# Kernel optimization log

Hardware: AMD Instinct MI355X
Metric: run time of the kernel (lower is better)

The kernel has to match this reference:

```python
import jax, jax.numpy as jnp
import numpy as np

L, D = 2, 128
NV, NF, E, G = 100000, 100000, 800000, 64


def setup_inputs() -> dict:
    key = jax.random.key(0)
    ks = jax.random.split(key, 16)
    p = lambda k, s: (0.02 * jax.random.normal(k, s)).astype(jnp.float32)
    return {
        "variables": jax.random.normal(ks[0], (NV, D), jnp.float32),
        "factors": jax.random.normal(ks[1], (NF, D), jnp.float32),
        "edge_index": jnp.stack([
            jax.random.randint(ks[2], (E,), 0, NV),
            jax.random.randint(ks[3], (E,), 0, NF),
        ]).astype(jnp.int64 if jax.config.jax_enable_x64 else jnp.int32),
        "edge_attr": jax.random.normal(ks[4], (E,), jnp.float32),
        "batch_idx": jnp.sort(jax.random.randint(ks[5], (NF,), 0, G)),
        "Wm_vf": p(ks[6], (L, 2 * D, D)), "bm_vf": jnp.zeros((L, D), jnp.float32),
        "Wc_vf": p(ks[7], (L, 2 * D, D)), "bc_vf": jnp.zeros((L, D), jnp.float32),
        "Wm_fv": p(ks[8], (L, 2 * D, D)), "bm_fv": jnp.zeros((L, D), jnp.float32),
        "Wc_fv": p(ks[9], (L, 2 * D, D)), "bc_fv": jnp.zeros((L, D), jnp.float32),
        "Wg": p(ks[10], (D, 1)), "bg": jnp.zeros((1,), jnp.float32),
        "Wt": p(ks[11], (D, D)), "bt": jnp.zeros((D,), jnp.float32),
        "Wl": p(ks[12], (2 * D, D)), "bl": jnp.zeros((D,), jnp.float32),
    }


def _mlp(x, W, b):
    # MLPLayer assumed = Linear + activation (relu)
    return jax.nn.relu(x @ W + b)


def reference(variables, factors, edge_index, edge_attr, batch_idx,
              Wm_vf, bm_vf, Wc_vf, bc_vf, Wm_fv, bm_fv, Wc_fv, bc_fv,
              Wg, bg, Wt, bt, Wl, bl):
    src_v = edge_index[0]  # variable index per edge
    dst_f = edge_index[1]  # factor index per edge
    for l in range(L):
        # var -> factor: message MLP(concat[x_i=factor@dst, x_j=var@src]), sum-agg into factors
        m_vf = _mlp(jnp.concatenate([factors[dst_f], variables[src_v]], -1), Wm_vf[l], bm_vf[l])
        aggr_f = jax.ops.segment_sum(m_vf, dst_f, num_segments=NF)
        new_factors = _mlp(jnp.concatenate([factors, aggr_f], -1), Wc_vf[l], bc_vf[l])
        # factor -> var (flipped edges): message MLP(concat[x_i=var@src_v, x_j=factor@dst_f])
        m_fv = _mlp(jnp.concatenate([variables[src_v], factors[dst_f]], -1), Wm_fv[l], bm_fv[l])
        aggr_v = jax.ops.segment_sum(m_fv, src_v, num_segments=NV)
        new_variables = variables + _mlp(jnp.concatenate([variables, aggr_v], -1), Wc_fv[l], bc_fv[l])
        variables, factors = new_variables, new_factors
    # GlobalNode: attentional aggregation over factors, g_prev = zeros
    gate = (factors @ Wg + bg)[:, 0]                                  # [NF]
    seg_max = jax.ops.segment_max(gate, batch_idx, num_segments=G)
    e = jnp.exp(gate - seg_max[batch_idx])
    denom = jax.ops.segment_sum(e, batch_idx, num_segments=G)
    attn = e / denom[batch_idx]                                       # segment softmax
    g_att = jax.ops.segment_sum(attn[:, None] * (factors @ Wt + bt), batch_idx, num_segments=G)
    g_prev = jnp.zeros((G, D), factors.dtype)
    g = g_prev + _mlp(jnp.concatenate([g_att, g_prev], -1), Wl, bl)
    return variables, factors, g
```

## Files before the change

kernel.cpp:

```cpp
#include <hip/hip_runtime.h>
#include <hip/hip_bf16.h>

typedef unsigned short u16;
typedef unsigned int u32;
typedef __attribute__((ext_vector_type(4))) float f32x4;
typedef __attribute__((ext_vector_type(8))) __bf16 bf16x8;

__device__ __forceinline__ u16 f2bf(float f) {
    u32 x = __float_as_uint(f);
    u32 r = x + 0x7fffu + ((x >> 16) & 1u);
    return (u16)(r >> 16);
}
__device__ __forceinline__ float bf2f(u16 u) {
    return __uint_as_float(((u32)u) << 16);
}

__global__ __launch_bounds__(256) void prep_w(
    const float* __restrict__ Wm_vf, const float* __restrict__ Wc_vf,
    const float* __restrict__ Wm_fv, const float* __restrict__ Wc_fv,
    const float* __restrict__ Wtr, u16* __restrict__ dst)
{
    int i = blockIdx.x * 256 + threadIdx.x;
    if (i >= 17 * 16384) return;
    int m = i >> 14;
    int r = i & 16383;
    int c = r >> 7;
    int k = r & 127;
    const float* p;
    if (m == 16) {
        p = Wtr;
    } else {
        int l = m >> 3, j = m & 7;
        const float* base = (j < 2) ? Wm_vf : (j < 4) ? Wm_fv : (j < 6) ? Wc_vf : Wc_fv;
        p = base + l * 32768 + (j & 1) * 16384;
    }
    dst[m * 16384 + c * 128 + k] = f2bf(p[k * 128 + c]);
}

#define EPB 2048

__global__ __launch_bounds__(256) void hist_part(
    const int* __restrict__ es, const int* __restrict__ ed,
    int* __restrict__ cntV, int* __restrict__ cntF,
    int E, int vChunk, int fChunk)
{
    int part = blockIdx.x & 7;
    int base = (blockIdx.x >> 3) * EPB;
    int end = base + EPB < E ? base + EPB : E;
    int vLo = part * vChunk, vHi = vLo + vChunk;
    int fLo = part * fChunk, fHi = fLo + fChunk;
    for (int i = base + threadIdx.x; i < end; i += 256) {
        int v = es[i], f = ed[i];
        if (v >= vLo && v < vHi) atomicAdd(&cntV[v], 1);
        if (f >= fLo && f < fHi) atomicAdd(&cntF[f], 1);
    }
}

__global__ __launch_bounds__(256) void scan1_k(
    const int* __restrict__ cnt, int* __restrict__ rs, int* __restrict__ bsum, int N)
{
    __shared__ int sd[256];
    int t = threadIdx.x;
    int b0 = blockIdx.x * 1024;
    int v[4]; int s = 0;
#pragma unroll
    for (int j = 0; j < 4; j++) { int i = b0 + t * 4 + j; v[j] = (i < N) ? cnt[i] : 0; s += v[j]; }
    sd[t] = s; __syncthreads();
    for (int off = 1; off < 256; off <<= 1) {
        int x = (t >= off) ? sd[t - off] : 0;
        __syncthreads();
        sd[t] += x;
        __syncthreads();
    }
    int excl = sd[t] - s;
    if (t == 255) bsum[blockIdx.x] = sd[255];
    int run = excl;
#pragma unroll
    for (int j = 0; j < 4; j++) { int i = b0 + t * 4 + j; if (i < N) rs[i] = run; run += v[j]; }
}

__global__ __launch_bounds__(256) void scan2_k(int* __restrict__ bsum, int NB)
{
    __shared__ int sd[256];
    int t = threadIdx.x;
    int s = (t < NB) ? bsum[t] : 0;
    sd[t] = s; __syncthreads();
    for (int off = 1; off < 256; off <<= 1) {
        int x = (t >= off) ? sd[t - off] : 0;
        __syncthreads();
        sd[t] += x;
        __syncthreads();
    }
    if (t < NB) bsum[t] = sd[t] - s;
}

__global__ __launch_bounds__(256) void scan3_k(
    int* __restrict__ rs, const int* __restrict__ bsum, int N, int E)
{
    int i = blockIdx.x * 256 + threadIdx.x;
    if (i < N) rs[i] += bsum[i >> 10];
    else if (i == N) rs[N] = E;
}

__global__ __launch_bounds__(256) void fill_part(
    const int* __restrict__ es, const int* __restrict__ ed,
    const int* __restrict__ rsF, const int* __restrict__ rsV,
    int* __restrict__ cntF, int* __restrict__ cntV,
    int* __restrict__ elF, int* __restrict__ elV,
    int E, int vChunk, int fChunk)
{
    int part = blockIdx.x & 7;
    int base = (blockIdx.x >> 3) * EPB;
    int end = base + EPB < E ? base + EPB : E;
    int vLo = part * vChunk, vHi = vLo + vChunk;
    int fLo = part * fChunk, fHi = fLo + fChunk;
    for (int i = base + threadIdx.x; i < end; i += 256) {
        int v = es[i], f = ed[i];
        if (f >= fLo && f < fHi) { int p = rsF[f] + atomicSub(&cntF[f], 1) - 1; elF[p] = v; }
        if (v >= vLo && v < vHi) { int p = rsV[v] + atomicSub(&cntV[v], 1) - 1; elV[p] = f; }
    }
}

__global__ __launch_bounds__(256) void aggregate_k(
    u16* __restrict__ OWN, const u16* __restrict__ OTH,
    const int* __restrict__ rs, const int* __restrict__ el,
    const float* __restrict__ bias, int N)
{
    int row = blockIdx.x * 4 + (threadIdx.x >> 6);
    if (row >= N) return;
    int lane = threadIdx.x & 63;
    int start = rs[row], end = rs[row + 1];
    ushort2 h = *(const ushort2*)&OWN[(size_t)row * 128 + lane * 2];
    float2 bv = *(const float2*)&bias[lane * 2];
    float c0 = bf2f(h.x) + bv.x;
    float c1 = bf2f(h.y) + bv.y;
    float a0 = 0.f, a1 = 0.f;
    for (int p0 = start; p0 < end; p0 += 64) {
        int n = end - p0; if (n > 64) n = 64;
        int myidx = (lane < n) ? el[p0 + lane] : 0;
        int j = 0;
        for (; j + 4 <= n; j += 4) {
            int o0 = __shfl(myidx, j);
            int o1 = __shfl(myidx, j + 1);
            int o2 = __shfl(myidx, j + 2);
            int o3 = __shfl(myidx, j + 3);
            ushort2 b0 = *(const ushort2*)&OTH[(size_t)o0 * 128 + lane * 2];
            ushort2 b1 = *(const ushort2*)&OTH[(size_t)o1 * 128 + lane * 2];
            ushort2 b2 = *(const ushort2*)&OTH[(size_t)o2 * 128 + lane * 2];
            ushort2 b3 = *(const ushort2*)&OTH[(size_t)o3 * 128 + lane * 2];
            a0 += fmaxf(c0 + bf2f(b0.x), 0.f) + fmaxf(c0 + bf2f(b1.x), 0.f)
                + fmaxf(c0 + bf2f(b2.x), 0.f) + fmaxf(c0 + bf2f(b3.x), 0.f);
            a1 += fmaxf(c1 + bf2f(b0.y), 0.f) + fmaxf(c1 + bf2f(b1.y), 0.f)
                + fmaxf(c1 + bf2f(b2.y), 0.f) + fmaxf(c1 + bf2f(b3.y), 0.f);
        }
        for (; j < n; j++) {
            int o = __shfl(myidx, j);
            ushort2 b = *(const ushort2*)&OTH[(size_t)o * 128 + lane * 2];
            a0 += fmaxf(c0 + bf2f(b.x), 0.f);
            a1 += fmaxf(c1 + bf2f(b.y), 0.f);
        }
    }
    ushort2 r; r.x = f2bf(a0); r.y = f2bf(a1);
    *(ushort2*)&OWN[(size_t)row * 128 + lane * 2] = r;
}

template <bool TWO, bool X2BF, bool RELU, bool RES, bool OBF16>
__global__ __launch_bounds__(256) void gemm_k(
    const float* __restrict__ X1, const void* __restrict__ X2,
    const u16* __restrict__ W1, const u16* __restrict__ W2,
    const float* __restrict__ bias, const float* __restrict__ res,
    float* __restrict__ Yf, u16* __restrict__ Yb, int N)
{
    __shared__ __align__(16) u16 Xs[64 * 136];
    __shared__ __align__(16) u16 Ws[128 * 136];
    const int tid = threadIdx.x;
    const int lane = tid & 63;
    const int wv = tid >> 6;
    const int r0 = blockIdx.x * 64;

    f32x4 acc[8];
#pragma unroll
    for (int i = 0; i < 8; i++) acc[i] = (f32x4)0.f;

#pragma unroll
    for (int p = 0; p < (TWO ? 2 : 1); ++p) {
        const u16* __restrict__ W = (TWO && p) ? W2 : W1;
        if (p) __syncthreads();
        if (TWO && p && X2BF) {
            const u16* Xb = (const u16*)X2;
#pragma unroll
            for (int j = 0; j < 4; j++) {
                int q = j * 256 + tid;
                int row = q >> 4;
                int col = (q & 15) * 8;
                uint4 v = make_uint4(0, 0, 0, 0);
                int gr = r0 + row;
                if (gr < N) v = *(const uint4*)&Xb[(size_t)gr * 128 + col];
                *(uint4*)&Xs[row * 136 + col] = v;
            }
        } else {
            const float* __restrict__ X = (TWO && p) ? (const float*)X2 : X1;
#pragma unroll
            for (int j = 0; j < 8; j++) {
                int q = j * 256 + tid;
                int row = q >> 5;
                int col = (q & 31) * 4;
                float4 v = make_float4(0.f, 0.f, 0.f, 0.f);
                int gr = r0 + row;
                if (gr < N) v = *(const float4*)&X[(size_t)gr * 128 + col];
                ushort4 h;
                h.x = f2bf(v.x); h.y = f2bf(v.y); h.z = f2bf(v.z); h.w = f2bf(v.w);
                *(ushort4*)&Xs[row * 136 + col] = h;
            }
        }
#pragma unroll
        for (int j = 0; j < 8; j++) {
            int q = j * 256 + tid;
            int c = q >> 4;
            int k = (q & 15) * 8;
            uint4 w = *(const uint4*)&W[c * 128 + k];
            *(uint4*)&Ws[c * 136 + k] = w;
        }
        __syncthreads();
#pragma unroll
        for (int ks = 0; ks < 4; ks++) {
            bf16x8 a = *(const bf16x8*)&Xs[(wv * 16 + (lane & 15)) * 136 + ks * 32 + (lane >> 4) * 8];
#pragma unroll
            for (int ct = 0; ct < 8; ct++) {
                bf16x8 b = *(const bf16x8*)&Ws[(ct * 16 + (lane & 15)) * 136 + ks * 32 + (lane >> 4) * 8];
                acc[ct] = __builtin_amdgcn_mfma_f32_16x16x32_bf16(a, b, acc[ct], 0, 0, 0);
            }
        }
    }
#pragma unroll
    for (int ct = 0; ct < 8; ct++) {
        int col = ct * 16 + (lane & 15);
        float bv = bias ? bias[col] : 0.f;
#pragma unroll
        for (int r = 0; r < 4; r++) {
            int row = wv * 16 + (lane >> 4) * 4 + r;
            int gr = r0 + row;
            if (gr < N) {
                float v = acc[ct][r] + bv;
                if (RELU) v = fmaxf(v, 0.f);
                if (RES) v += res[(size_t)gr * 128 + col];
                if (OBF16) Yb[(size_t)gr * 128 + col] = f2bf(v);
                else       Yf[(size_t)gr * 128 + col] = v;
            }
        }
    }
}

__global__ __launch_bounds__(256) void gemm_dual(
    const float* __restrict__ X, const u16* __restrict__ W1, const u16* __restrict__ W2,
    u16* __restrict__ Y1, u16* __restrict__ Y2, int N)
{
    __shared__ __align__(16) u16 Xs[64 * 136];
    __shared__ __align__(16) u16 Ws[128 * 136];
    const int tid = threadIdx.x;
    const int lane = tid & 63;
    const int wv = tid >> 6;
    const int r0 = blockIdx.x * 64;

    f32x4 acc1[8], acc2[8];
#pragma unroll
    for (int i = 0; i < 8; i++) { acc1[i] = (f32x4)0.f; acc2[i] = (f32x4)0.f; }

#pragma unroll
    for (int j = 0; j < 8; j++) {
        int q = j * 256 + tid;
        int row = q >> 5;
        int col = (q & 31) * 4;
        float4 v = make_float4(0.f, 0.f, 0.f, 0.f);
        int gr = r0 + row;
        if (gr < N) v = *(const float4*)&X[(size_t)gr * 128 + col];
        ushort4 h;
        h.x = f2bf(v.x); h.y = f2bf(v.y); h.z = f2bf(v.z); h.w = f2bf(v.w);
        *(ushort4*)&Xs[row * 136 + col] = h;
    }
#pragma unroll
    for (int p = 0; p < 2; ++p) {
        const u16* __restrict__ W = p ? W2 : W1;
        if (p) __syncthreads();
#pragma unroll
        for (int j = 0; j < 8; j++) {
            int q = j * 256 + tid;
            int c = q >> 4;
            int k = (q & 15) * 8;
            uint4 w = *(const uint4*)&W[c * 128 + k];
            *(uint4*)&Ws[c * 136 + k] = w;
        }
        __syncthreads();
#pragma unroll
        for (int ks = 0; ks < 4; ks++) {
            bf16x8 a = *(const bf16x8*)&Xs[(wv * 16 + (lane & 15)) * 136 + ks * 32 + (lane >> 4) * 8];
#pragma unroll
            for (int ct = 0; ct < 8; ct++) {
                bf16x8 b = *(const bf16x8*)&Ws[(ct * 16 + (lane & 15)) * 136 + ks * 32 + (lane >> 4) * 8];
                if (p) acc2[ct] = __builtin_amdgcn_mfma_f32_16x16x32_bf16(a, b, acc2[ct], 0, 0, 0);
                else   acc1[ct] = __builtin_amdgcn_mfma_f32_16x16x32_bf16(a, b, acc1[ct], 0, 0, 0);
            }
        }
    }
#pragma unroll
    for (int ct = 0; ct < 8; ct++) {
        int col = ct * 16 + (lane & 15);
#pragma unroll
        for (int r = 0; r < 4; r++) {
            int row = wv * 16 + (lane >> 4) * 4 + r;
            int gr = r0 + row;
            if (gr < N) {
                Y1[(size_t)gr * 128 + col] = f2bf(acc1[ct][r]);
                Y2[(size_t)gr * 128 + col] = f2bf(acc2[ct][r]);
            }
        }
    }
}

__global__ __launch_bounds__(256) void gate_k(
    const float* __restrict__ F, const float* __restrict__ Wg,
    const float* __restrict__ bg, float* __restrict__ gate, int NF)
{
    int lane = threadIdx.x & 63;
    int f = blockIdx.x * 4 + (threadIdx.x >> 6);
    if (f >= NF) return;
    float p = F[(size_t)f * 128 + lane] * Wg[lane]
            + F[(size_t)f * 128 + 64 + lane] * Wg[64 + lane];
#pragma unroll
    for (int off = 32; off; off >>= 1) p += __shfl_down(p, off);
    if (lane == 0) gate[f] = p + bg[0];
}

__global__ __launch_bounds__(256) void gstats_k(
    const float* __restrict__ gate, const int* __restrict__ batch,
    float* __restrict__ mx, float* __restrict__ dn, int NF)
{
    int g = blockIdx.x, tid = threadIdx.x;
    int lo = 0, hi = NF;
    while (lo < hi) { int mid = (lo + hi) >> 1; if (batch[mid] < g) lo = mid + 1; else hi = mid; }
    int start = lo;
    lo = start; hi = NF;
    while (lo < hi) { int mid = (lo + hi) >> 1; if (batch[mid] < g + 1) lo = mid + 1; else hi = mid; }
    int end = lo;

    __shared__ float red[256];
    float m = -3.4e38f;
    for (int i = start + tid; i < end; i += 256) m = fmaxf(m, gate[i]);
    red[tid] = m; __syncthreads();
    for (int s = 128; s; s >>= 1) { if (tid < s) red[tid] = fmaxf(red[tid], red[tid + s]); __syncthreads(); }
    float mval = red[0]; __syncthreads();
    float s = 0.f;
    for (int i = start + tid; i < end; i += 256) s += __expf(gate[i] - mval);
    red[tid] = s; __syncthreads();
    for (int t = 128; t; t >>= 1) { if (tid < t) red[tid] += red[tid + t]; __syncthreads(); }
    if (tid == 0) { mx[g] = mval; dn[g] = red[0]; }
}

__global__ __launch_bounds__(128) void wsum_k(
    const float* __restrict__ gate, const float* __restrict__ T,
    const int* __restrict__ batch, const float* __restrict__ mx,
    const float* __restrict__ dn, float* __restrict__ g_att, int NF)
{
    int tid = threadIdx.x;
    int i0 = blockIdx.x * 256;
    if (i0 >= NF) return;
    int iend = i0 + 256; if (iend > NF) iend = NF;
    int curg = batch[i0];
    float acc = 0.f;
    for (int i = i0; i < iend; i++) {
        int g = batch[i];
        if (g != curg) {
            atomicAdd(&g_att[(size_t)curg * 128 + tid], acc);
            acc = 0.f; curg = g;
        }
        float w = __expf(gate[i] - mx[g]) / dn[g];
        acc += w * T[(size_t)i * 128 + tid];
    }
    atomicAdd(&g_att[(size_t)curg * 128 + tid], acc);
}

__global__ __launch_bounds__(128) void gfinal_k(
    const float* __restrict__ g_att, const float* __restrict__ Wl,
    const float* __restrict__ bl, float* __restrict__ out_g)
{
    int g = blockIdx.x, tid = threadIdx.x;
    __shared__ float ga[128];
    ga[tid] = g_att[(size_t)g * 128 + tid];
    __syncthreads();
    float o = bl[tid];
    for (int k = 0; k < 128; k++) o += ga[k] * Wl[k * 128 + tid];
    out_g[(size_t)g * 128 + tid] = fmaxf(o, 0.f);
}

extern "C" void kernel_launch(void* const* d_in, const int* in_sizes, int n_in,
                              void* d_out, int out_size, void* d_ws, size_t ws_size,
                              hipStream_t stream)
{
    const int D = 128;
    const int NV = in_sizes[0] / D;
    const int NF = in_sizes[1] / D;
    const int E  = in_sizes[2] / 2;
    const int G  = out_size / D - NV - NF;

    const float* vars_in = (const float*)d_in[0];
    const float* facs_in = (const float*)d_in[1];
    const int*   eidx    = (const int*)d_in[2];
    const int*   e_src   = eidx;
    const int*   e_dst   = eidx + E;
    const int*   batch   = (const int*)d_in[4];
    const float* Wm_vf = (const float*)d_in[5],  *bm_vf = (const float*)d_in[6];
    const float* Wc_vf = (const float*)d_in[7],  *bc_vf = (const float*)d_in[8];
    const float* Wm_fv = (const float*)d_in[9],  *bm_fv = (const float*)d_in[10];
    const float* Wc_fv = (const float*)d_in[11], *bc_fv = (const float*)d_in[12];
    const float* Wg  = (const float*)d_in[13], *bg = (const float*)d_in[14];
    const float* Wtr = (const float*)d_in[15], *bt = (const float*)d_in[16];
    const float* Wl  = (const float*)d_in[17], *bl = (const float*)d_in[18];

    char* ws = (char*)d_ws;
    size_t off = 0;
    u16* WB   = (u16*)ws;            off = 1u << 20;
    u16* BUFA = (u16*)(ws + off);    off += (size_t)NF * 256;
    u16* BUFB = (u16*)(ws + off);    off += (size_t)NV * 256;
    u16* BUFC = (u16*)(ws + off);    off += (size_t)NF * 256;
    float* Tbuf = (float*)BUFA;
    int* rsF  = (int*)(ws + off);    off += (size_t)(NF + 1) * 4;
    int* rsV  = (int*)(ws + off);    off += (size_t)(NV + 1) * 4;
    int* cntF = (int*)(ws + off);    off += (size_t)NF * 4;
    int* cntV = (int*)(ws + off);    off += (size_t)NV * 4;
    int* elF  = (int*)(ws + off);    off += (size_t)E * 4;
    int* elV  = (int*)(ws + off);    off += (size_t)E * 4;
    int* bsum = (int*)(ws + off);    off += 4096;
    float* mx    = (float*)(ws + off); off += (size_t)G * 4;
    float* dn    = (float*)(ws + off); off += (size_t)G * 4;
    float* g_att = (float*)(ws + off); off += (size_t)G * 512;
    float* gate  = (float*)(ws + off); off += (size_t)NF * 4;

    float* out_v = (float*)d_out;
    float* out_f = out_v + (size_t)NV * D;
    float* out_g = out_f + (size_t)NF * D;

    prep_w<<<(17 * 16384 + 255) / 256, 256, 0, stream>>>(Wm_vf, Wc_vf, Wm_fv, Wc_fv, Wtr, WB);

    const int vChunk = (NV + 7) / 8, fChunk = (NF + 7) / 8;
    const int CH = (E + EPB - 1) / EPB;
    hipMemsetAsync(cntF, 0, (size_t)(NF + NV) * 4, stream);
    hist_part<<<CH * 8, 256, 0, stream>>>(e_src, e_dst, cntV, cntF, E, vChunk, fChunk);
    const int NBf = (NF + 1023) / 1024, NBv = (NV + 1023) / 1024;
    scan1_k<<<NBf, 256, 0, stream>>>(cntF, rsF, bsum, NF);
    scan2_k<<<1, 256, 0, stream>>>(bsum, NBf);
    scan3_k<<<(NF + 256) / 256, 256, 0, stream>>>(rsF, bsum, NF, E);
    scan1_k<<<NBv, 256, 0, stream>>>(cntV, rsV, bsum, NV);
    scan2_k<<<1, 256, 0, stream>>>(bsum, NBv);
    scan3_k<<<(NV + 256) / 256, 256, 0, stream>>>(rsV, bsum, NV, E);
    fill_part<<<CH * 8, 256, 0, stream>>>(e_src, e_dst, rsF, rsV, cntF, cntV, elF, elV, E, vChunk, fChunk);

    const int GBv = (NV + 63) / 64;
    const int GBf = (NF + 63) / 64;
    const int GAf = (NF + 3) / 4;
    const int GAv = (NV + 3) / 4;

    for (int l = 0; l < 2; l++) {
        u16* wb = WB + l * 8 * 16384;
        const float* Fin = l ? out_f : facs_in;
        const float* Vin = l ? out_v : vars_in;
        gemm_dual<<<GBf, 256, 0, stream>>>(Fin, wb + 0 * 16384, wb + 3 * 16384, BUFA, BUFC, NF);
        gemm_k<false, false, false, false, true><<<GBv, 256, 0, stream>>>(
            Vin, nullptr, wb + 1 * 16384, nullptr, nullptr, nullptr, nullptr, BUFB, NV);
        aggregate_k<<<GAf, 256, 0, stream>>>(BUFA, BUFB, rsF, elF, bm_vf + l * D, NF);
        gemm_k<true, true, true, false, false><<<GBf, 256, 0, stream>>>(
            Fin, BUFA, wb + 4 * 16384, wb + 5 * 16384, bc_vf + l * D, nullptr, out_f, nullptr, NF);
        gemm_k<false, false, false, false, true><<<GBv, 256, 0, stream>>>(
            Vin, nullptr, wb + 2 * 16384, nullptr, nullptr, nullptr, nullptr, BUFB, NV);
        aggregate_k<<<GAv, 256, 0, stream>>>(BUFB, BUFC, rsV, elV, bm_fv + l * D, NV);
        gemm_k<true, true, true, true, false><<<GBv, 256, 0, stream>>>(
            Vin, BUFB, wb + 6 * 16384, wb + 7 * 16384, bc_fv + l * D, Vin, out_v, nullptr, NV);
    }

    gemm_k<false, false, false, false, false><<<GBf, 256, 0, stream>>>(
        out_f, nullptr, WB + 16 * 16384, nullptr, bt, nullptr, Tbuf, nullptr, NF);
    gate_k<<<(NF + 3) / 4, 256, 0, stream>>>(out_f, Wg, bg, gate, NF);
    gstats_k<<<G, 256, 0, stream>>>(gate, batch, mx, dn, NF);
    hipMemsetAsync(g_att, 0, (size_t)G * 512, stream);
    wsum_k<<<(NF + 255) / 256, 128, 0, stream>>>(gate, Tbuf, batch, mx, dn, g_att, NF);
    gfinal_k<<<G, 128, 0, stream>>>(g_att, Wl, bl, out_g);
}
```

Baseline: 1.019 ms.

## Fuse projection GEMMs, fold gate into factor GEMM, move Wt after pooling

Merges the factor dual-projection and the variable projection into one launch, and likewise fuses the factor combine GEMM with the next variable projection. The gate dot product moves into the last-layer factor combine epilogue. Because attention weights sum to one per segment, the Wt transform is applied to the pooled features in gfinal_k instead of per factor, which removes a full NF×128 GEMM. Also normalises attention in place, shrinks wsum blocks for more parallelism, and unrolls the aggregation gather by 8. The Wt reordering changes the rounding path (fp32 on pooled values instead of bf16 per row) and needs special handling for empty segments.

```diff
diff --git a/kernel.cpp b/kernel.cpp
--- a/kernel.cpp
+++ b/kernel.cpp
@@ -18,22 +18,17 @@
 __global__ __launch_bounds__(256) void prep_w(
     const float* __restrict__ Wm_vf, const float* __restrict__ Wc_vf,
     const float* __restrict__ Wm_fv, const float* __restrict__ Wc_fv,
-    const float* __restrict__ Wtr, u16* __restrict__ dst)
+    u16* __restrict__ dst)
 {
     int i = blockIdx.x * 256 + threadIdx.x;
-    if (i >= 17 * 16384) return;
+    if (i >= 16 * 16384) return;
     int m = i >> 14;
     int r = i & 16383;
     int c = r >> 7;
     int k = r & 127;
-    const float* p;
-    if (m == 16) {
-        p = Wtr;
-    } else {
-        int l = m >> 3, j = m & 7;
-        const float* base = (j < 2) ? Wm_vf : (j < 4) ? Wm_fv : (j < 6) ? Wc_vf : Wc_fv;
-        p = base + l * 32768 + (j & 1) * 16384;
-    }
+    int l = m >> 3, j = m & 7;
+    const float* base = (j < 2) ? Wm_vf : (j < 4) ? Wm_fv : (j < 6) ? Wc_vf : Wc_fv;
+    const float* p = base + l * 32768 + (j & 1) * 16384;
     dst[m * 16384 + c * 128 + k] = f2bf(p[k * 128 + c]);
 }
 
@@ -139,23 +134,36 @@
         int n = end - p0; if (n > 64) n = 64;
         int myidx = (lane < n) ? el[p0 + lane] : 0;
         int j = 0;
+        for (; j + 8 <= n; j += 8) {
+            ushort2 b0 = *(const ushort2*)&OTH[(size_t)__shfl(myidx, j)     * 128 + lane * 2];
+            ushort2 b1 = *(const ushort2*)&OTH[(size_t)__shfl(myidx, j + 1) * 128 + lane * 2];
+            ushort2 b2 = *(const ushort2*)&OTH[(size_t)__shfl(myidx, j + 2) * 128 + lane * 2];
+            ushort2 b3 = *(const ushort2*)&OTH[(size_t)__shfl(myidx, j + 3) * 128 + lane * 2];
+            ushort2 b4 = *(const ushort2*)&OTH[(size_t)__shfl(myidx, j + 4) * 128 + lane * 2];
+            ushort2 b5 = *(const ushort2*)&OTH[(size_t)__shfl(myidx, j + 5) * 128 + lane * 2];
+            ushort2 b6 = *(const ushort2*)&OTH[(size_t)__shfl(myidx, j + 6) * 128 + lane * 2];
+            ushort2 b7 = *(const ushort2*)&OTH[(size_t)__shfl(myidx, j + 7) * 128 + lane * 2];
+            a0 += fmaxf(c0 + bf2f(b0.x), 0.f) + fmaxf(c0 + bf2f(b1.x), 0.f)
+                + fmaxf(c0 + bf2f(b2.x), 0.f) + fmaxf(c0 + bf2f(b3.x), 0.f)
+                + fmaxf(c0 + bf2f(b4.x), 0.f) + fmaxf(c0 + bf2f(b5.x), 0.f)
+                + fmaxf(c0 + bf2f(b6.x), 0.f) + fmaxf(c0 + bf2f(b7.x), 0.f);
+            a1 += fmaxf(c1 + bf2f(b0.y), 0.f) + fmaxf(c1 + bf2f(b1.y), 0.f)
+                + fmaxf(c1 + bf2f(b2.y), 0.f) + fmaxf(c1 + bf2f(b3.y), 0.f)
+                + fmaxf(c1 + bf2f(b4.y), 0.f) + fmaxf(c1 + bf2f(b5.y), 0.f)
+                + fmaxf(c1 + bf2f(b6.y), 0.f) + fmaxf(c1 + bf2f(b7.y), 0.f);
+        }
         for (; j + 4 <= n; j += 4) {
-            int o0 = __shfl(myidx, j);
-            int o1 = __shfl(myidx, j + 1);
-            int o2 = __shfl(myidx, j + 2);
-            int o3 = __shfl(myidx, j + 3);
-            ushort2 b0 = *(const ushort2*)&OTH[(size_t)o0 * 128 + lane * 2];
-            ushort2 b1 = *(const ushort2*)&OTH[(size_t)o1 * 128 + lane * 2];
-            ushort2 b2 = *(const ushort2*)&OTH[(size_t)o2 * 128 + lane * 2];
-            ushort2 b3 = *(const ushort2*)&OTH[(size_t)o3 * 128 + lane * 2];
+            ushort2 b0 = *(const ushort2*)&OTH[(size_t)__shfl(myidx, j)     * 128 + lane * 2];
+            ushort2 b1 = *(const ushort2*)&OTH[(size_t)__shfl(myidx, j + 1) * 128 + lane * 2];
+            ushort2 b2 = *(const ushort2*)&OTH[(size_t)__shfl(myidx, j + 2) * 128 + lane * 2];
+            ushort2 b3 = *(const ushort2*)&OTH[(size_t)__shfl(myidx, j + 3) * 128 + lane * 2];
             a0 += fmaxf(c0 + bf2f(b0.x), 0.f) + fmaxf(c0 + bf2f(b1.x), 0.f)
                 + fmaxf(c0 + bf2f(b2.x), 0.f) + fmaxf(c0 + bf2f(b3.x), 0.f);
             a1 += fmaxf(c1 + bf2f(b0.y), 0.f) + fmaxf(c1 + bf2f(b1.y), 0.f)
                 + fmaxf(c1 + bf2f(b2.y), 0.f) + fmaxf(c1 + bf2f(b3.y), 0.f);
         }
         for (; j < n; j++) {
-            int o = __shfl(myidx, j);
-            ushort2 b = *(const ushort2*)&OTH[(size_t)o * 128 + lane * 2];
+            ushort2 b = *(const ushort2*)&OTH[(size_t)__shfl(myidx, j) * 128 + lane * 2];
             a0 += fmaxf(c0 + bf2f(b.x), 0.f);
             a1 += fmaxf(c1 + bf2f(b.y), 0.f);
         }
@@ -164,108 +172,9 @@
     *(ushort2*)&OWN[(size_t)row * 128 + lane * 2] = r;
 }
 
-template <bool TWO, bool X2BF, bool RELU, bool RES, bool OBF16>
-__global__ __launch_bounds__(256) void gemm_k(
-    const float* __restrict__ X1, const void* __restrict__ X2,
-    const u16* __restrict__ W1, const u16* __restrict__ W2,
-    const float* __restrict__ bias, const float* __restrict__ res,
-    float* __restrict__ Yf, u16* __restrict__ Yb, int N)
-{
-    __shared__ __align__(16) u16 Xs[64 * 136];
-    __shared__ __align__(16) u16 Ws[128 * 136];
-    const int tid = threadIdx.x;
-    const int lane = tid & 63;
-    const int wv = tid >> 6;
-    const int r0 = blockIdx.x * 64;
-
-    f32x4 acc[8];
-#pragma unroll
-    for (int i = 0; i < 8; i++) acc[i] = (f32x4)0.f;
-
-#pragma unroll
-    for (int p = 0; p < (TWO ? 2 : 1); ++p) {
-        const u16* __restrict__ W = (TWO && p) ? W2 : W1;
-        if (p) __syncthreads();
-        if (TWO && p && X2BF) {
-            const u16* Xb = (const u16*)X2;
-#pragma unroll
-            for (int j = 0; j < 4; j++) {
-                int q = j * 256 + tid;
-                int row = q >> 4;
-                int col = (q & 15) * 8;
-                uint4 v = make_uint4(0, 0, 0, 0);
-                int gr = r0 + row;
-                if (gr < N) v = *(const uint4*)&Xb[(size_t)gr * 128 + col];
-                *(uint4*)&Xs[row * 136 + col] = v;
-            }
-        } else {
-            const float* __restrict__ X = (TWO && p) ? (const float*)X2 : X1;
-#pragma unroll
-            for (int j = 0; j < 8; j++) {
-                int q = j * 256 + tid;
-                int row = q >> 5;
-                int col = (q & 31) * 4;
-                float4 v = make_float4(0.f, 0.f, 0.f, 0.f);
-                int gr = r0 + row;
-                if (gr < N) v = *(const float4*)&X[(size_t)gr * 128 + col];
-                ushort4 h;
-                h.x = f2bf(v.x); h.y = f2bf(v.y); h.z = f2bf(v.z); h.w = f2bf(v.w);
-                *(ushort4*)&Xs[row * 136 + col] = h;
-            }
-        }
-#pragma unroll
-        for (int j = 0; j < 8; j++) {
-            int q = j * 256 + tid;
-            int c = q >> 4;
-            int k = (q & 15) * 8;
-            uint4 w = *(const uint4*)&W[c * 128 + k];
-            *(uint4*)&Ws[c * 136 + k] = w;
-        }
-        __syncthreads();
-#pragma unroll
-        for (int ks = 0; ks < 4; ks++) {
-            bf16x8 a = *(const bf16x8*)&Xs[(wv * 16 + (lane & 15)) * 136 + ks * 32 + (lane >> 4) * 8];
-#pragma unroll
-            for (int ct = 0; ct < 8; ct++) {
-                bf16x8 b = *(const bf16x8*)&Ws[(ct * 16 + (lane & 15)) * 136 + ks * 32 + (lane >> 4) * 8];
-                acc[ct] = __builtin_amdgcn_mfma_f32_16x16x32_bf16(a, b, acc[ct], 0, 0, 0);
-            }
-        }
-    }
-#pragma unroll
-    for (int ct = 0; ct < 8; ct++) {
-        int col = ct * 16 + (lane & 15);
-        float bv = bias ? bias[col] : 0.f;
-#pragma unroll
-        for (int r = 0; r < 4; r++) {
-            int row = wv * 16 + (lane >> 4) * 4 + r;
-            int gr = r0 + row;
-            if (gr < N) {
-                float v = acc[ct][r] + bv;
-                if (RELU) v = fmaxf(v, 0.f);
-                if (RES) v += res[(size_t)gr * 128 + col];
-                if (OBF16) Yb[(size_t)gr * 128 + col] = f2bf(v);
-                else       Yf[(size_t)gr * 128 + col] = v;
-            }
-        }
-    }
-}
-
-__global__ __launch_bounds__(256) void gemm_dual(
-    const float* __restrict__ X, const u16* __restrict__ W1, const u16* __restrict__ W2,
-    u16* __restrict__ Y1, u16* __restrict__ Y2, int N)
-{
-    __shared__ __align__(16) u16 Xs[64 * 136];
-    __shared__ __align__(16) u16 Ws[128 * 136];
-    const int tid = threadIdx.x;
-    const int lane = tid & 63;
-    const int wv = tid >> 6;
-    const int r0 = blockIdx.x * 64;
-
-    f32x4 acc1[8], acc2[8];
-#pragma unroll
-    for (int i = 0; i < 8; i++) { acc1[i] = (f32x4)0.f; acc2[i] = (f32x4)0.f; }
-
+__device__ __forceinline__ void stage_Xf(const float* __restrict__ X, int r0, int N,
+                                         u16* __restrict__ Xs, int tid)
+{
 #pragma unroll
     for (int j = 0; j < 8; j++) {
         int q = j * 256 + tid;
@@ -278,62 +187,220 @@
         h.x = f2bf(v.x); h.y = f2bf(v.y); h.z = f2bf(v.z); h.w = f2bf(v.w);
         *(ushort4*)&Xs[row * 136 + col] = h;
     }
-#pragma unroll
-    for (int p = 0; p < 2; ++p) {
-        const u16* __restrict__ W = p ? W2 : W1;
-        if (p) __syncthreads();
-#pragma unroll
-        for (int j = 0; j < 8; j++) {
-            int q = j * 256 + tid;
-            int c = q >> 4;
-            int k = (q & 15) * 8;
-            uint4 w = *(const uint4*)&W[c * 128 + k];
-            *(uint4*)&Ws[c * 136 + k] = w;
-        }
-        __syncthreads();
-#pragma unroll
-        for (int ks = 0; ks < 4; ks++) {
-            bf16x8 a = *(const bf16x8*)&Xs[(wv * 16 + (lane & 15)) * 136 + ks * 32 + (lane >> 4) * 8];
-#pragma unroll
-            for (int ct = 0; ct < 8; ct++) {
-                bf16x8 b = *(const bf16x8*)&Ws[(ct * 16 + (lane & 15)) * 136 + ks * 32 + (lane >> 4) * 8];
-                if (p) acc2[ct] = __builtin_amdgcn_mfma_f32_16x16x32_bf16(a, b, acc2[ct], 0, 0, 0);
-                else   acc1[ct] = __builtin_amdgcn_mfma_f32_16x16x32_bf16(a, b, acc1[ct], 0, 0, 0);
-            }
-        }
-    }
+}
+__device__ __forceinline__ void stage_Xb(const u16* __restrict__ X, int r0, int N,
+                                         u16* __restrict__ Xs, int tid)
+{
+#pragma unroll
+    for (int j = 0; j < 4; j++) {
+        int q = j * 256 + tid;
+        int row = q >> 4;
+        int col = (q & 15) * 8;
+        uint4 v = make_uint4(0, 0, 0, 0);
+        int gr = r0 + row;
+        if (gr < N) v = *(const uint4*)&X[(size_t)gr * 128 + col];
+        *(uint4*)&Xs[row * 136 + col] = v;
+    }
+}
+__device__ __forceinline__ void stage_W(const u16* __restrict__ W, u16* __restrict__ Ws, int tid)
+{
+#pragma unroll
+    for (int j = 0; j < 8; j++) {
+        int q = j * 256 + tid;
+        int c = q >> 4;
+        int k = (q & 15) * 8;
+        *(uint4*)&Ws[c * 136 + k] = *(const uint4*)&W[c * 128 + k];
+    }
+}
+__device__ __forceinline__ void mfma8(const u16* __restrict__ Xs, const u16* __restrict__ Ws,
+                                      int lane, int wv, f32x4* acc)
+{
+#pragma unroll
+    for (int ks = 0; ks < 4; ks++) {
+        bf16x8 a = *(const bf16x8*)&Xs[(wv * 16 + (lane & 15)) * 136 + ks * 32 + (lane >> 4) * 8];
+#pragma unroll
+        for (int ct = 0; ct < 8; ct++) {
+            bf16x8 b = *(const bf16x8*)&Ws[(ct * 16 + (lane & 15)) * 136 + ks * 32 + (lane >> 4) * 8];
+            acc[ct] = __builtin_amdgcn_mfma_f32_16x16x32_bf16(a, b, acc[ct], 0, 0, 0);
+        }
+    }
+}
+
+__global__ __launch_bounds__(256) void proj3_k(
+    const float* __restrict__ F, const float* __restrict__ V,
+    const u16* __restrict__ W0, const u16* __restrict__ W3, const u16* __restrict__ W1,
+    u16* __restrict__ BUFA, u16* __restrict__ BUFC, u16* __restrict__ BUFB,
+    int NF, int NV, int GBf)
+{
+    __shared__ __align__(16) u16 Xs[64 * 136];
+    __shared__ __align__(16) u16 Ws[128 * 136];
+    const int tid = threadIdx.x, lane = tid & 63, wv = tid >> 6;
+    if ((int)blockIdx.x < GBf) {
+        const int r0 = blockIdx.x * 64;
+        f32x4 acc1[8], acc2[8];
+#pragma unroll
+        for (int i = 0; i < 8; i++) { acc1[i] = (f32x4)0.f; acc2[i] = (f32x4)0.f; }
+        stage_Xf(F, r0, NF, Xs, tid);
+        stage_W(W0, Ws, tid);
+        __syncthreads();
+        mfma8(Xs, Ws, lane, wv, acc1);
+        __syncthreads();
+        stage_W(W3, Ws, tid);
+        __syncthreads();
+        mfma8(Xs, Ws, lane, wv, acc2);
+#pragma unroll
+        for (int ct = 0; ct < 8; ct++) {
+            int col = ct * 16 + (lane & 15);
+#pragma unroll
+            for (int r = 0; r < 4; r++) {
+                int gr = r0 + wv * 16 + (lane >> 4) * 4 + r;
+                if (gr < NF) {
+                    BUFA[(size_t)gr * 128 + col] = f2bf(acc1[ct][r]);
+                    BUFC[(size_t)gr * 128 + col] = f2bf(acc2[ct][r]);
+                }
+            }
+        }
+    } else {
+        const int r0 = (blockIdx.x - GBf) * 64;
+        f32x4 acc[8];
+#pragma unroll
+        for (int i = 0; i < 8; i++) acc[i] = (f32x4)0.f;
+        stage_Xf(V, r0, NV, Xs, tid);
+        stage_W(W1, Ws, tid);
+        __syncthreads();
+        mfma8(Xs, Ws, lane, wv, acc);
+#pragma unroll
+        for (int ct = 0; ct < 8; ct++) {
+            int col = ct * 16 + (lane & 15);
+#pragma unroll
+            for (int r = 0; r < 4; r++) {
+                int gr = r0 + wv * 16 + (lane >> 4) * 4 + r;
+                if (gr < NV) BUFB[(size_t)gr * 128 + col] = f2bf(acc[ct][r]);
+            }
+        }
+    }
+}
+
+template <bool GATE>
+__global__ __launch_bounds__(256) void mixF_k(
+    const float* __restrict__ Fin, const u16* __restrict__ AGG,
+    const u16* __restrict__ W4, const u16* __restrict__ W5,
+    const float* __restrict__ bc, float* __restrict__ out_f,
+    const float* __restrict__ Vin, const u16* __restrict__ W2,
+    u16* __restrict__ BUFB,
+    const float* __restrict__ Wg, const float* __restrict__ bg,
+    float* __restrict__ gate, int NF, int NV, int GBf)
+{
+    __shared__ __align__(16) u16 Xs[64 * 136];
+    __shared__ __align__(16) u16 Ws[128 * 136];
+    const int tid = threadIdx.x, lane = tid & 63, wv = tid >> 6;
+    if ((int)blockIdx.x < GBf) {
+        const int r0 = blockIdx.x * 64;
+        f32x4 acc[8];
+#pragma unroll
+        for (int i = 0; i < 8; i++) acc[i] = (f32x4)0.f;
+        stage_Xf(Fin, r0, NF, Xs, tid);
+        stage_W(W4, Ws, tid);
+        __syncthreads();
+        mfma8(Xs, Ws, lane, wv, acc);
+        __syncthreads();
+        stage_Xb(AGG, r0, NF, Xs, tid);
+        stage_W(W5, Ws, tid);
+        __syncthreads();
+        mfma8(Xs, Ws, lane, wv, acc);
+        float gp[4] = {0.f, 0.f, 0.f, 0.f};
+#pragma unroll
+        for (int ct = 0; ct < 8; ct++) {
+            int col = ct * 16 + (lane & 15);
+            float bv = bc[col];
+            float wgv = GATE ? Wg[col] : 0.f;
+#pragma unroll
+            for (int r = 0; r < 4; r++) {
+                int gr = r0 + wv * 16 + (lane >> 4) * 4 + r;
+                if (gr < NF) {
+                    float v = fmaxf(acc[ct][r] + bv, 0.f);
+                    out_f[(size_t)gr * 128 + col] = v;
+                    if (GATE) gp[r] += v * wgv;
+                }
+            }
+        }
+        if (GATE) {
+#pragma unroll
+            for (int r = 0; r < 4; r++) {
+                gp[r] += __shfl_xor(gp[r], 1);
+                gp[r] += __shfl_xor(gp[r], 2);
+                gp[r] += __shfl_xor(gp[r], 4);
+                gp[r] += __shfl_xor(gp[r], 8);
+            }
+            if ((lane & 15) == 0) {
+                float b0 = bg[0];
+#pragma unroll
+                for (int r = 0; r < 4; r++) {
+                    int gr = r0 + wv * 16 + (lane >> 4) * 4 + r;
+                    if (gr < NF) gate[gr] = gp[r] + b0;
+                }
+            }
+        }
+    } else {
+        const int r0 = (blockIdx.x - GBf) * 64;
+        f32x4 acc[8];
+#pragma unroll
+        for (int i = 0; i < 8; i++) acc[i] = (f32x4)0.f;
+        stage_Xf(Vin, r0, NV, Xs, tid);
+        stage_W(W2, Ws, tid);
+        __syncthreads();
+        mfma8(Xs, Ws, lane, wv, acc);
+#pragma unroll
+        for (int ct = 0; ct < 8; ct++) {
+            int col = ct * 16 + (lane & 15);
+#pragma unroll
+            for (int r = 0; r < 4; r++) {
+                int gr = r0 + wv * 16 + (lane >> 4) * 4 + r;
+                if (gr < NV) BUFB[(size_t)gr * 128 + col] = f2bf(acc[ct][r]);
+            }
+        }
+    }
+}
+
+__global__ __launch_bounds__(256) void combineV_k(
+    const float* __restrict__ Vin, const u16* __restrict__ AGG,
+    const u16* __restrict__ W6, const u16* __restrict__ W7,
+    const float* __restrict__ bc, float* __restrict__ out_v, int NV)
+{
+    __shared__ __align__(16) u16 Xs[64 * 136];
+    __shared__ __align__(16) u16 Ws[128 * 136];
+    const int tid = threadIdx.x, lane = tid & 63, wv = tid >> 6;
+    const int r0 = blockIdx.x * 64;
+    f32x4 acc[8];
+#pragma unroll
+    for (int i = 0; i < 8; i++) acc[i] = (f32x4)0.f;
+    stage_Xf(Vin, r0, NV, Xs, tid);
+    stage_W(W6, Ws, tid);
+    __syncthreads();
+    mfma8(Xs, Ws, lane, wv, acc);
+    __syncthreads();
+    stage_Xb(AGG, r0, NV, Xs, tid);
+    stage_W(W7, Ws, tid);
+    __syncthreads();
+    mfma8(Xs, Ws, lane, wv, acc);
 #pragma unroll
     for (int ct = 0; ct < 8; ct++) {
         int col = ct * 16 + (lane & 15);
+        float bv = bc[col];
 #pragma unroll
         for (int r = 0; r < 4; r++) {
-            int row = wv * 16 + (lane >> 4) * 4 + r;
-            int gr = r0 + row;
-            if (gr < N) {
-                Y1[(size_t)gr * 128 + col] = f2bf(acc1[ct][r]);
-                Y2[(size_t)gr * 128 + col] = f2bf(acc2[ct][r]);
-            }
-        }
-    }
-}
-
-__global__ __launch_bounds__(256) void gate_k(
-    const float* __restrict__ F, const float* __restrict__ Wg,
-    const float* __restrict__ bg, float* __restrict__ gate, int NF)
-{
-    int lane = threadIdx.x & 63;
-    int f = blockIdx.x * 4 + (threadIdx.x >> 6);
-    if (f >= NF) return;
-    float p = F[(size_t)f * 128 + lane] * Wg[lane]
-            + F[(size_t)f * 128 + 64 + lane] * Wg[64 + lane];
-#pragma unroll
-    for (int off = 32; off; off >>= 1) p += __shfl_down(p, off);
-    if (lane == 0) gate[f] = p + bg[0];
+            int gr = r0 + wv * 16 + (lane >> 4) * 4 + r;
+            if (gr < NV) {
+                float v = fmaxf(acc[ct][r] + bv, 0.f) + Vin[(size_t)gr * 128 + col];
+                out_v[(size_t)gr * 128 + col] = v;
+            }
+        }
+    }
 }
 
 __global__ __launch_bounds__(256) void gstats_k(
-    const float* __restrict__ gate, const int* __restrict__ batch,
-    float* __restrict__ mx, float* __restrict__ dn, int NF)
+    float* __restrict__ gate, const int* __restrict__ batch,
+    float* __restrict__ dn, int NF)
 {
     int g = blockIdx.x, tid = threadIdx.x;
     int lo = 0, hi = NF;
@@ -350,21 +417,27 @@
     for (int s = 128; s; s >>= 1) { if (tid < s) red[tid] = fmaxf(red[tid], red[tid + s]); __syncthreads(); }
     float mval = red[0]; __syncthreads();
     float s = 0.f;
-    for (int i = start + tid; i < end; i += 256) s += __expf(gate[i] - mval);
+    for (int i = start + tid; i < end; i += 256) {
+        float e = __expf(gate[i] - mval);
+        gate[i] = e;
+        s += e;
+    }
     red[tid] = s; __syncthreads();
     for (int t = 128; t; t >>= 1) { if (tid < t) red[tid] += red[tid + t]; __syncthreads(); }
-    if (tid == 0) { mx[g] = mval; dn[g] = red[0]; }
+    float denom = red[0];
+    if (tid == 0) dn[g] = denom;
+    float rdn = (denom > 0.f) ? 1.f / denom : 0.f;
+    for (int i = start + tid; i < end; i += 256) gate[i] *= rdn;
 }
 
 __global__ __launch_bounds__(128) void wsum_k(
-    const float* __restrict__ gate, const float* __restrict__ T,
-    const int* __restrict__ batch, const float* __restrict__ mx,
-    const float* __restrict__ dn, float* __restrict__ g_att, int NF)
+    const float* __restrict__ attn, const float* __restrict__ F,
+    const int* __restrict__ batch, float* __restrict__ g_att, int NF)
 {
     int tid = threadIdx.x;
-    int i0 = blockIdx.x * 256;
+    int i0 = blockIdx.x * 32;
     if (i0 >= NF) return;
-    int iend = i0 + 256; if (iend > NF) iend = NF;
+    int iend = i0 + 32; if (iend > NF) iend = NF;
     int curg = batch[i0];
     float acc = 0.f;
     for (int i = i0; i < iend; i++) {
@@ -373,22 +446,28 @@
             atomicAdd(&g_att[(size_t)curg * 128 + tid], acc);
             acc = 0.f; curg = g;
         }
-        float w = __expf(gate[i] - mx[g]) / dn[g];
-        acc += w * T[(size_t)i * 128 + tid];
+        acc += attn[i] * F[(size_t)i * 128 + tid];
     }
     atomicAdd(&g_att[(size_t)curg * 128 + tid], acc);
 }
 
 __global__ __launch_bounds__(128) void gfinal_k(
-    const float* __restrict__ g_att, const float* __restrict__ Wl,
-    const float* __restrict__ bl, float* __restrict__ out_g)
+    const float* __restrict__ g_att, const float* __restrict__ dn,
+    const float* __restrict__ Wt, const float* __restrict__ bt,
+    const float* __restrict__ Wl, const float* __restrict__ bl,
+    float* __restrict__ out_g)
 {
     int g = blockIdx.x, tid = threadIdx.x;
-    __shared__ float ga[128];
+    __shared__ float ga[128], tt[128];
     ga[tid] = g_att[(size_t)g * 128 + tid];
     __syncthreads();
+    float t = 0.f;
+    for (int k = 0; k < 128; k++) t += ga[k] * Wt[k * 128 + tid];
+    bool nonempty = dn[g] > 0.f;
+    t = nonempty ? t + bt[tid] : 0.f;
+    tt[tid] = t; __syncthreads();
     float o = bl[tid];
-    for (int k = 0; k < 128; k++) o += ga[k] * Wl[k * 128 + tid];
+    for (int k = 0; k < 128; k++) o += tt[k] * Wl[k * 128 + tid];
     out_g[(size_t)g * 128 + tid] = fmaxf(o, 0.f);
 }
 
@@ -422,7 +501,6 @@
     u16* BUFA = (u16*)(ws + off);    off += (size_t)NF * 256;
     u16* BUFB = (u16*)(ws + off);    off += (size_t)NV * 256;
     u16* BUFC = (u16*)(ws + off);    off += (size_t)NF * 256;
-    float* Tbuf = (float*)BUFA;
     int* rsF  = (int*)(ws + off);    off += (size_t)(NF + 1) * 4;
     int* rsV  = (int*)(ws + off);    off += (size_t)(NV + 1) * 4;
     int* cntF = (int*)(ws + off);    off += (size_t)NF * 4;
@@ -430,7 +508,6 @@
     int* elF  = (int*)(ws + off);    off += (size_t)E * 4;
     int* elV  = (int*)(ws + off);    off += (size_t)E * 4;
     int* bsum = (int*)(ws + off);    off += 4096;
-    float* mx    = (float*)(ws + off); off += (size_t)G * 4;
     float* dn    = (float*)(ws + off); off += (size_t)G * 4;
     float* g_att = (float*)(ws + off); off += (size_t)G * 512;
     float* gate  = (float*)(ws + off); off += (size_t)NF * 4;
@@ -439,7 +516,7 @@
     float* out_f = out_v + (size_t)NV * D;
     float* out_g = out_f + (size_t)NF * D;
 
-    prep_w<<<(17 * 16384 + 255) / 256, 256, 0, stream>>>(Wm_vf, Wc_vf, Wm_fv, Wc_fv, Wtr, WB);
+    prep_w<<<(16 * 16384 + 255) / 256, 256, 0, stream>>>(Wm_vf, Wc_vf, Wm_fv, Wc_fv, WB);
 
     const int vChunk = (NV + 7) / 8, fChunk = (NF + 7) / 8;
     const int CH = (E + EPB - 1) / EPB;
@@ -463,24 +540,25 @@
         u16* wb = WB + l * 8 * 16384;
         const float* Fin = l ? out_f : facs_in;
         const float* Vin = l ? out_v : vars_in;
-        gemm_dual<<<GBf, 256, 0, stream>>>(Fin, wb + 0 * 16384, wb + 3 * 16384, BUFA, BUFC, NF);
-        gemm_k<false, false, false, false, true><<<GBv, 256, 0, stream>>>(
-            Vin, nullptr, wb + 1 * 16384, nullptr, nullptr, nullptr, nullptr, BUFB, NV);
+        proj3_k<<<GBf + GBv, 256, 0, stream>>>(
+            Fin, Vin, wb + 0 * 16384, wb + 3 * 16384, wb + 1 * 16384,
+            BUFA, BUFC, BUFB, NF, NV, GBf);
         aggregate_k<<<GAf, 256, 0, stream>>>(BUFA, BUFB, rsF, elF, bm_vf + l * D, NF);
-        gemm_k<true, true, true, false, false><<<GBf, 256, 0, stream>>>(
-            Fin, BUFA, wb + 4 * 16384, wb + 5 * 16384, bc_vf + l * D, nullptr, out_f, nullptr, NF);
-        gemm_k<false, false, false, false, true><<<GBv, 256, 0, stream>>>(
-            Vin, nullptr, wb + 2 * 16384, nullptr, nullptr, nullptr, nullptr, BUFB, NV);
+        if (l == 0)
+            mixF_k<false><<<GBf + GBv, 256, 0, stream>>>(
+                Fin, BUFA, wb + 4 * 16384, wb + 5 * 16384, bc_vf + l * D, out_f,
+                Vin, wb + 2 * 16384, BUFB, nullptr, nullptr, nullptr, NF, NV, GBf);
+        else
+            mixF_k<true><<<GBf + GBv, 256, 0, stream>>>(
+                Fin, BUFA, wb + 4 * 16384, wb + 5 * 16384, bc_vf + l * D, out_f,
+                Vin, wb + 2 * 16384, BUFB, Wg, bg, gate, NF, NV, GBf);
         aggregate_k<<<GAv, 256, 0, stream>>>(BUFB, BUFC, rsV, elV, bm_fv + l * D, NV);
-        gemm_k<true, true, true, true, false><<<GBv, 256, 0, stream>>>(
-            Vin, BUFB, wb + 6 * 16384, wb + 7 * 16384, bc_fv + l * D, Vin, out_v, nullptr, NV);
-    }
-
-    gemm_k<false, false, false, false, false><<<GBf, 256, 0, stream>>>(
-        out_f, nullptr, WB + 16 * 16384, nullptr, bt, nullptr, Tbuf, nullptr, NF);
-    gate_k<<<(NF + 3) / 4, 256, 0, stream>>>(out_f, Wg, bg, gate, NF);
-    gstats_k<<<G, 256, 0, stream>>>(gate, batch, mx, dn, NF);
+        combineV_k<<<GBv, 256, 0, stream>>>(
+            Vin, BUFB, wb + 6 * 16384, wb + 7 * 16384, bc_fv + l * D, out_v, NV);
+    }
+
+    gstats_k<<<G, 256, 0, stream>>>(gate, batch, dn, NF);
     hipMemsetAsync(g_att, 0, (size_t)G * 512, stream);
-    wsum_k<<<(NF + 255) / 256, 128, 0, stream>>>(gate, Tbuf, batch, mx, dn, g_att, NF);
-    gfinal_k<<<G, 128, 0, stream>>>(g_att, Wl, bl, out_g);
-}
+    wsum_k<<<(NF + 31) / 32, 128, 0, stream>>>(gate, out_f, batch, g_att, NF);
+    gfinal_k<<<G, 128, 0, stream>>>(g_att, dn, Wtr, bt, Wl, bl, out_g);
+}
```

After: 840.2 us. -17.6%, faster.
